# Performance work log

Measured on AMD Instinct MI355X. Metric: run time of the kernel, lower is better.

## Reference

```python
import jax, jax.numpy as jnp
import numpy as np

ALPHA = 1.702  # sigmoid-GLU scale
LIMIT = 7.0    # clamp limit
TOP_K = 2      # num_experts_per_tok


def setup_inputs() -> dict:
    key = jax.random.key(0)
    ks = jax.random.split(key, 4)
    B, S, H, E, I = 2, 1024, 1024, 8, 2048
    return {
        "hidden_states": jax.random.normal(ks[0], (B, S, H), jnp.float32),
        "router_weight": jax.random.normal(ks[1], (E, H), jnp.float32),
        "router_bias": jnp.zeros((E,), jnp.float32),
        "gate_up_proj": jax.random.normal(ks[2], (E, H, 2 * I), jnp.float32) * 0.02,
        "gate_up_bias": jnp.zeros((E, 2 * I), jnp.float32),
        "down_proj": jax.random.normal(ks[3], (E, I, H), jnp.float32) * 0.02,
        "down_bias": jnp.zeros((E, H), jnp.float32),
    }


def reference(hidden_states, router_weight, router_bias, gate_up_proj,
              gate_up_bias, down_proj, down_bias):
    B, S, H = hidden_states.shape
    E, _, two_I = gate_up_proj.shape
    I = two_I // 2

    flat = hidden_states.reshape(B * S, H)  # [T, H]

    # Router: softmax + top-k
    logits = flat @ router_weight.T + router_bias            # [T, E]
    scores = jax.nn.softmax(logits, axis=-1)
    topk_w, topk_idx = jax.lax.top_k(scores, TOP_K)          # [T, K]

    # Dense per-expert gated FFN (einsum 'abmh,ehn->abemn' computes all experts
    # on all tokens; the reshape/permute dance is a mathematical no-op).
    gu = jnp.einsum('th,ehn->ten', flat, gate_up_proj) + gate_up_bias  # [T, E, 2I]
    gate = jnp.minimum(gu[..., :I], LIMIT)
    up = jnp.clip(gu[..., I:], -LIMIT, LIMIT)
    glu = gate * jax.nn.sigmoid(gate * ALPHA)
    act = (up + 1.0) * glu                                   # [T, E, I]

    down = jnp.einsum('tei,eih->teh', act, down_proj) + down_bias  # [T, E, H]

    # Combine: gather each token's top-k expert outputs, weighted sum.
    gathered = jnp.take_along_axis(down, topk_idx[:, :, None], axis=1)  # [T, K, H]
    out = (gathered * topk_w[:, :, None]).sum(axis=1)        # [T, H]
    return out.reshape(B, S, H)
```

## Files before the change

### kernel.cpp

```cpp
#include <hip/hip_runtime.h>
#include <math.h>

#define TT 2048
#define HH 1024
#define EE 8
#define II 2048
#define N1 4096
#define ALPHA 1.702f
#define LIMIT 7.0f

typedef __attribute__((ext_vector_type(8))) short short8;
typedef __attribute__((ext_vector_type(4))) float floatx4;

__device__ __forceinline__ short f2bf(float f) {
  union { float f; unsigned u; } v; v.f = f;
  unsigned r = (v.u + 0x7fffu + ((v.u >> 16) & 1u)) >> 16;
  return (short)r;
}
__device__ __forceinline__ float bf2f(unsigned short s) {
  union { unsigned u; float f; } v; v.u = ((unsigned)s) << 16;
  return v.f;
}

__global__ __launch_bounds__(256) void router_kernel(
    const float* __restrict__ x, const float* __restrict__ rw,
    const float* __restrict__ rb, int* __restrict__ topk_idx,
    float* __restrict__ topk_w) {
  const int t = blockIdx.x;
  const float* xr = x + (size_t)t * HH;
  const int lane = threadIdx.x & 63;
  const int wave = threadIdx.x >> 6;
  float xv[16];
#pragma unroll
  for (int i = 0; i < 16; i++) xv[i] = xr[lane + i * 64];
  __shared__ float logits[EE];
#pragma unroll
  for (int ee = 0; ee < 2; ee++) {
    const int e = wave * 2 + ee;
    const float* wr = rw + (size_t)e * HH;
    float s = 0.f;
#pragma unroll
    for (int i = 0; i < 16; i++) s += xv[i] * wr[lane + i * 64];
#pragma unroll
    for (int off = 32; off > 0; off >>= 1) s += __shfl_down(s, off, 64);
    if (lane == 0) logits[e] = s + rb[e];
  }
  __syncthreads();
  if (threadIdx.x == 0) {
    float l[EE], sc[EE];
    float mx = -3.4e38f;
    for (int i = 0; i < EE; i++) { l[i] = logits[i]; mx = fmaxf(mx, l[i]); }
    float sum = 0.f;
    for (int i = 0; i < EE; i++) { sc[i] = expf(l[i] - mx); sum += sc[i]; }
    const float inv = 1.f / sum;
    int i0 = 0;
    for (int i = 1; i < EE; i++) if (sc[i] > sc[i0]) i0 = i;
    int i1 = (i0 == 0) ? 1 : 0;
    for (int i = 0; i < EE; i++) if (i != i0 && sc[i] > sc[i1]) i1 = i;
    topk_idx[t * 2 + 0] = i0;
    topk_idx[t * 2 + 1] = i1;
    topk_w[t * 2 + 0] = sc[i0] * inv;
    topk_w[t * 2 + 1] = sc[i1] * inv;
  }
}

__global__ void assign_kernel(const int* __restrict__ topk_idx,
                              int* __restrict__ counts, int* __restrict__ rows) {
  const int id = blockIdx.x * blockDim.x + threadIdx.x;
  if (id >= TT * 2) return;
  const int e = topk_idx[id];
  const int slot = atomicAdd(&counts[e], 1);
  rows[e * TT + slot] = id;
}

__global__ __launch_bounds__(256) void gemm_gu(
    const float* __restrict__ x, const float* __restrict__ gup,
    const float* __restrict__ gub, const int* __restrict__ counts,
    const int* __restrict__ rows, unsigned short* __restrict__ gu) {
  const int e = blockIdx.z, mtile = blockIdx.y, ntile = blockIdx.x;
  const int count = counts[e];
  if (mtile * 128 >= count) return;
  const int* rl = rows + e * TT + mtile * 128;
  __shared__ short As[128][40];
  __shared__ short Bs[128][40];
  const int tid = threadIdx.x;
  const int lane = tid & 63, wave = tid >> 6;
  const int wm = (wave & 1) << 6, wn = (wave >> 1) << 6;
  const int quad = lane >> 4, r16 = lane & 15;

  const int arow = tid >> 2, akoct = tid & 3;
  const int cr0 = (mtile * 128 + arow < count) ? arow : (count - 1 - mtile * 128);
  const int cr1 = (mtile * 128 + arow + 64 < count) ? arow + 64 : (count - 1 - mtile * 128);
  const float* a0 = x + (size_t)(rl[cr0] >> 1) * HH;
  const float* a1 = x + (size_t)(rl[cr1] >> 1) * HH;

  const int bn = tid & 127, bk = tid >> 7;
  const float* bb = gup + (size_t)e * HH * N1 + ntile * 128 + bn;

  floatx4 acc[4][4] = {};

  for (int k0 = 0; k0 < HH; k0 += 32) {
    __syncthreads();
    {
      const float4* p = (const float4*)(a0 + k0 + akoct * 8);
      float4 v0 = p[0], v1 = p[1];
      short8 s;
      s[0]=f2bf(v0.x); s[1]=f2bf(v0.y); s[2]=f2bf(v0.z); s[3]=f2bf(v0.w);
      s[4]=f2bf(v1.x); s[5]=f2bf(v1.y); s[6]=f2bf(v1.z); s[7]=f2bf(v1.w);
      *(short8*)&As[arow][akoct * 8] = s;
      p = (const float4*)(a1 + k0 + akoct * 8);
      v0 = p[0]; v1 = p[1];
      s[0]=f2bf(v0.x); s[1]=f2bf(v0.y); s[2]=f2bf(v0.z); s[3]=f2bf(v0.w);
      s[4]=f2bf(v1.x); s[5]=f2bf(v1.y); s[6]=f2bf(v1.z); s[7]=f2bf(v1.w);
      *(short8*)&As[arow + 64][akoct * 8] = s;
    }
    {
      const float* p = bb + (size_t)(k0 + bk * 8) * N1;
      short8 s;
#pragma unroll
      for (int j = 0; j < 8; j++) s[j] = f2bf(p[(size_t)j * N1]);
      *(short8*)&Bs[bn][bk * 8] = s;
      p = bb + (size_t)(k0 + (bk + 2) * 8) * N1;
#pragma unroll
      for (int j = 0; j < 8; j++) s[j] = f2bf(p[(size_t)j * N1]);
      *(short8*)&Bs[bn][(bk + 2) * 8] = s;
    }
    __syncthreads();
    short8 af[4], bf_[4];
#pragma unroll
    for (int i = 0; i < 4; i++)
      af[i] = *(const short8*)&As[wm + i * 16 + r16][quad * 8];
#pragma unroll
    for (int j = 0; j < 4; j++)
      bf_[j] = *(const short8*)&Bs[wn + j * 16 + r16][quad * 8];
#pragma unroll
    for (int i = 0; i < 4; i++)
#pragma unroll
      for (int j = 0; j < 4; j++)
        acc[i][j] = __builtin_amdgcn_mfma_f32_16x16x32_bf16(af[i], bf_[j], acc[i][j], 0, 0, 0);
  }
#pragma unroll
  for (int i = 0; i < 4; i++) {
#pragma unroll
    for (int reg = 0; reg < 4; reg++) {
      const int rrow = wm + i * 16 + quad * 4 + reg;
      if (mtile * 128 + rrow < count) {
        const int ent = rl[rrow];
        unsigned short* orow = gu + (size_t)ent * N1 + ntile * 128;
#pragma unroll
        for (int j = 0; j < 4; j++) {
          const int c = wn + j * 16 + r16;
          const float v = acc[i][j][reg] + gub[e * N1 + ntile * 128 + c];
          orow[c] = (unsigned short)f2bf(v);
        }
      }
    }
  }
}

__global__ void act_kernel(const unsigned short* __restrict__ gu,
                           unsigned short* __restrict__ act) {
  const int id = blockIdx.x * blockDim.x + threadIdx.x;
  if (id >= TT * 2 * II) return;
  const int r = id >> 11;
  const int i = id & (II - 1);
  float g = bf2f(gu[(size_t)r * N1 + i]);
  float u = bf2f(gu[(size_t)r * N1 + II + i]);
  g = fminf(g, LIMIT);
  u = fminf(fmaxf(u, -LIMIT), LIMIT);
  const float glu = g / (1.f + expf(-g * ALPHA));
  act[(size_t)r * II + i] = (unsigned short)f2bf((u + 1.f) * glu);
}

__global__ __launch_bounds__(256) void gemm_down(
    const unsigned short* __restrict__ act, const float* __restrict__ dp,
    const float* __restrict__ db, const int* __restrict__ counts,
    const int* __restrict__ rows, float* __restrict__ dout) {
  const int e = blockIdx.z, mtile = blockIdx.y, ntile = blockIdx.x;
  const int count = counts[e];
  if (mtile * 128 >= count) return;
  const int* rl = rows + e * TT + mtile * 128;
  __shared__ short As[128][40];
  __shared__ short Bs[128][40];
  const int tid = threadIdx.x;
  const int lane = tid & 63, wave = tid >> 6;
  const int wm = (wave & 1) << 6, wn = (wave >> 1) << 6;
  const int quad = lane >> 4, r16 = lane & 15;

  const int arow = tid >> 2, akoct = tid & 3;
  const int cr0 = (mtile * 128 + arow < count) ? arow : (count - 1 - mtile * 128);
  const int cr1 = (mtile * 128 + arow + 64 < count) ? arow + 64 : (count - 1 - mtile * 128);
  const unsigned short* a0 = act + (size_t)rl[cr0] * II;
  const unsigned short* a1 = act + (size_t)rl[cr1] * II;

  const int bn = tid & 127, bk = tid >> 7;
  const float* bb = dp + (size_t)e * II * HH + ntile * 128 + bn;

  floatx4 acc[4][4] = {};

  for (int k0 = 0; k0 < II; k0 += 32) {
    __syncthreads();
    {
      *(short8*)&As[arow][akoct * 8] = *(const short8*)(a0 + k0 + akoct * 8);
      *(short8*)&As[arow + 64][akoct * 8] = *(const short8*)(a1 + k0 + akoct * 8);
    }
    {
      const float* p = bb + (size_t)(k0 + bk * 8) * HH;
      short8 s;
#pragma unroll
      for (int j = 0; j < 8; j++) s[j] = f2bf(p[(size_t)j * HH]);
      *(short8*)&Bs[bn][bk * 8] = s;
      p = bb + (size_t)(k0 + (bk + 2) * 8) * HH;
#pragma unroll
      for (int j = 0; j < 8; j++) s[j] = f2bf(p[(size_t)j * HH]);
      *(short8*)&Bs[bn][(bk + 2) * 8] = s;
    }
    __syncthreads();
    short8 af[4], bf_[4];
#pragma unroll
    for (int i = 0; i < 4; i++)
      af[i] = *(const short8*)&As[wm + i * 16 + r16][quad * 8];
#pragma unroll
    for (int j = 0; j < 4; j++)
      bf_[j] = *(const short8*)&Bs[wn + j * 16 + r16][quad * 8];
#pragma unroll
    for (int i = 0; i < 4; i++)
#pragma unroll
      for (int j = 0; j < 4; j++)
        acc[i][j] = __builtin_amdgcn_mfma_f32_16x16x32_bf16(af[i], bf_[j], acc[i][j], 0, 0, 0);
  }
#pragma unroll
  for (int i = 0; i < 4; i++) {
#pragma unroll
    for (int reg = 0; reg < 4; reg++) {
      const int rrow = wm + i * 16 + quad * 4 + reg;
      if (mtile * 128 + rrow < count) {
        const int ent = rl[rrow];
        float* orow = dout + (size_t)ent * HH + ntile * 128;
#pragma unroll
        for (int j = 0; j < 4; j++) {
          const int c = wn + j * 16 + r16;
          orow[c] = acc[i][j][reg] + db[e * HH + ntile * 128 + c];
        }
      }
    }
  }
}

__global__ void combine_kernel(const float* __restrict__ dout,
                               const float* __restrict__ tw,
                               float* __restrict__ out) {
  const int id = blockIdx.x * blockDim.x + threadIdx.x;
  const int t = id >> 8;
  const int h = (id & 255) * 4;
  const float w0 = tw[t * 2], w1 = tw[t * 2 + 1];
  const float4 a = *(const float4*)(dout + (size_t)(2 * t) * HH + h);
  const float4 b = *(const float4*)(dout + (size_t)(2 * t + 1) * HH + h);
  float4 o;
  o.x = w0 * a.x + w1 * b.x;
  o.y = w0 * a.y + w1 * b.y;
  o.z = w0 * a.z + w1 * b.z;
  o.w = w0 * a.w + w1 * b.w;
  *(float4*)(out + (size_t)t * HH + h) = o;
}

extern "C" void kernel_launch(void* const* d_in, const int* in_sizes, int n_in,
                              void* d_out, int out_size, void* d_ws, size_t ws_size,
                              hipStream_t stream) {
  const float* x   = (const float*)d_in[0];
  const float* rw  = (const float*)d_in[1];
  const float* rb  = (const float*)d_in[2];
  const float* gup = (const float*)d_in[3];
  const float* gub = (const float*)d_in[4];
  const float* dp  = (const float*)d_in[5];
  const float* db  = (const float*)d_in[6];
  float* out = (float*)d_out;

  char* ws = (char*)d_ws;
  int*   topk_idx = (int*)(ws + 0);
  float* topk_w   = (float*)(ws + 16384);
  int*   counts   = (int*)(ws + 32768);
  int*   rows     = (int*)(ws + 33024);
  unsigned short* gu  = (unsigned short*)(ws + 131072);
  unsigned short* act = (unsigned short*)(ws + 131072 + 33554432);
  float* dout = (float*)(ws + 131072 + 33554432 + 16777216);

  router_kernel<<<TT, 256, 0, stream>>>(x, rw, rb, topk_idx, topk_w);
  hipMemsetAsync(counts, 0, 64, stream);
  assign_kernel<<<(TT * 2 + 255) / 256, 256, 0, stream>>>(topk_idx, counts, rows);
  gemm_gu<<<dim3(N1 / 128, TT / 128, EE), 256, 0, stream>>>(x, gup, gub, counts, rows, gu);
  act_kernel<<<(TT * 2 * II) / 256, 256, 0, stream>>>(gu, act);
  gemm_down<<<dim3(HH / 128, TT / 128, EE), 256, 0, stream>>>(act, dp, db, counts, rows, dout);
  combine_kernel<<<(TT * HH / 4) / 256, 256, 0, stream>>>(dout, topk_w, out);
}
```

Measured before the change: 454.3 us.

## Double-buffer GEMM loads in registers, use 512-thread blocks, split-K down GEMM

Both expert GEMMs now use 512-thread blocks with eight waves, each computing a 64x32 sub-tile. They prefetch the next K slice into registers while the current slice is staged in LDS, and they convert fp32 to bf16 with the packed v_cvt_pk_bf16_f32 instruction. The down GEMM is split into two K halves that write separate partial buffers, reusing the free gu region for the second one, and the combine kernel adds the two halves. The activation kernel is vectorised to process eight elements per thread. The aim is more parallelism and latency hiding, paid for with higher register pressure, an extra partial buffer read in combine, and more blocks in the down GEMM.

```diff
diff --git a/kernel.cpp b/kernel.cpp
--- a/kernel.cpp
+++ b/kernel.cpp
@@ -11,6 +11,7 @@
 
 typedef __attribute__((ext_vector_type(8))) short short8;
 typedef __attribute__((ext_vector_type(4))) float floatx4;
+typedef __attribute__((ext_vector_type(4))) unsigned int uintx4;
 
 __device__ __forceinline__ short f2bf(float f) {
   union { float f; unsigned u; } v; v.f = f;
@@ -20,6 +21,11 @@
 __device__ __forceinline__ float bf2f(unsigned short s) {
   union { unsigned u; float f; } v; v.u = ((unsigned)s) << 16;
   return v.f;
+}
+__device__ __forceinline__ unsigned cvt2(float lo, float hi) {
+  unsigned r;
+  asm("v_cvt_pk_bf16_f32 %0, %1, %2" : "=v"(r) : "v"(lo), "v"(hi));
+  return r;
 }
 
 __global__ __launch_bounds__(256) void router_kernel(
@@ -73,7 +79,7 @@
   rows[e * TT + slot] = id;
 }
 
-__global__ __launch_bounds__(256) void gemm_gu(
+__global__ __launch_bounds__(512, 4) void gemm_gu(
     const float* __restrict__ x, const float* __restrict__ gup,
     const float* __restrict__ gub, const int* __restrict__ counts,
     const int* __restrict__ rows, unsigned short* __restrict__ gu) {
@@ -85,58 +91,55 @@
   __shared__ short Bs[128][40];
   const int tid = threadIdx.x;
   const int lane = tid & 63, wave = tid >> 6;
-  const int wm = (wave & 1) << 6, wn = (wave >> 1) << 6;
+  const int wm = (wave & 1) << 6, wn = (wave >> 1) << 5;
   const int quad = lane >> 4, r16 = lane & 15;
 
   const int arow = tid >> 2, akoct = tid & 3;
-  const int cr0 = (mtile * 128 + arow < count) ? arow : (count - 1 - mtile * 128);
-  const int cr1 = (mtile * 128 + arow + 64 < count) ? arow + 64 : (count - 1 - mtile * 128);
-  const float* a0 = x + (size_t)(rl[cr0] >> 1) * HH;
-  const float* a1 = x + (size_t)(rl[cr1] >> 1) * HH;
-
-  const int bn = tid & 127, bk = tid >> 7;
-  const float* bb = gup + (size_t)e * HH * N1 + ntile * 128 + bn;
-
-  floatx4 acc[4][4] = {};
+  const int cr = (mtile * 128 + arow < count) ? arow : (count - 1 - mtile * 128);
+  const float* ap = x + (size_t)(rl[cr] >> 1) * HH + akoct * 8;
+
+  const int bn = tid & 127, bko = tid >> 7;
+  const float* bp = gup + (size_t)e * HH * N1 + (size_t)bko * 8 * N1 + ntile * 128 + bn;
+
+  floatx4 acc[4][2] = {};
+
+  float4 va0 = ((const float4*)ap)[0];
+  float4 va1 = ((const float4*)ap)[1];
+  float vb[8];
+#pragma unroll
+  for (int j = 0; j < 8; j++) vb[j] = bp[(size_t)j * N1];
+  ap += 32;
+  bp += (size_t)32 * N1;
 
   for (int k0 = 0; k0 < HH; k0 += 32) {
     __syncthreads();
-    {
-      const float4* p = (const float4*)(a0 + k0 + akoct * 8);
-      float4 v0 = p[0], v1 = p[1];
-      short8 s;
-      s[0]=f2bf(v0.x); s[1]=f2bf(v0.y); s[2]=f2bf(v0.z); s[3]=f2bf(v0.w);
-      s[4]=f2bf(v1.x); s[5]=f2bf(v1.y); s[6]=f2bf(v1.z); s[7]=f2bf(v1.w);
-      *(short8*)&As[arow][akoct * 8] = s;
-      p = (const float4*)(a1 + k0 + akoct * 8);
-      v0 = p[0]; v1 = p[1];
-      s[0]=f2bf(v0.x); s[1]=f2bf(v0.y); s[2]=f2bf(v0.z); s[3]=f2bf(v0.w);
-      s[4]=f2bf(v1.x); s[5]=f2bf(v1.y); s[6]=f2bf(v1.z); s[7]=f2bf(v1.w);
-      *(short8*)&As[arow + 64][akoct * 8] = s;
-    }
-    {
-      const float* p = bb + (size_t)(k0 + bk * 8) * N1;
-      short8 s;
-#pragma unroll
-      for (int j = 0; j < 8; j++) s[j] = f2bf(p[(size_t)j * N1]);
-      *(short8*)&Bs[bn][bk * 8] = s;
-      p = bb + (size_t)(k0 + (bk + 2) * 8) * N1;
-#pragma unroll
-      for (int j = 0; j < 8; j++) s[j] = f2bf(p[(size_t)j * N1]);
-      *(short8*)&Bs[bn][(bk + 2) * 8] = s;
+    uintx4 aw, bw;
+    aw[0] = cvt2(va0.x, va0.y); aw[1] = cvt2(va0.z, va0.w);
+    aw[2] = cvt2(va1.x, va1.y); aw[3] = cvt2(va1.z, va1.w);
+    bw[0] = cvt2(vb[0], vb[1]); bw[1] = cvt2(vb[2], vb[3]);
+    bw[2] = cvt2(vb[4], vb[5]); bw[3] = cvt2(vb[6], vb[7]);
+    *(uintx4*)&As[arow][akoct * 8] = aw;
+    *(uintx4*)&Bs[bn][bko * 8] = bw;
+    if (k0 + 32 < HH) {
+      va0 = ((const float4*)ap)[0];
+      va1 = ((const float4*)ap)[1];
+#pragma unroll
+      for (int j = 0; j < 8; j++) vb[j] = bp[(size_t)j * N1];
+      ap += 32;
+      bp += (size_t)32 * N1;
     }
     __syncthreads();
-    short8 af[4], bf_[4];
+    short8 af[4], bf_[2];
 #pragma unroll
     for (int i = 0; i < 4; i++)
       af[i] = *(const short8*)&As[wm + i * 16 + r16][quad * 8];
 #pragma unroll
-    for (int j = 0; j < 4; j++)
+    for (int j = 0; j < 2; j++)
       bf_[j] = *(const short8*)&Bs[wn + j * 16 + r16][quad * 8];
 #pragma unroll
     for (int i = 0; i < 4; i++)
 #pragma unroll
-      for (int j = 0; j < 4; j++)
+      for (int j = 0; j < 2; j++)
         acc[i][j] = __builtin_amdgcn_mfma_f32_16x16x32_bf16(af[i], bf_[j], acc[i][j], 0, 0, 0);
   }
 #pragma unroll
@@ -148,7 +151,7 @@
         const int ent = rl[rrow];
         unsigned short* orow = gu + (size_t)ent * N1 + ntile * 128;
 #pragma unroll
-        for (int j = 0; j < 4; j++) {
+        for (int j = 0; j < 2; j++) {
           const int c = wn + j * 16 + r16;
           const float v = acc[i][j][reg] + gub[e * N1 + ntile * 128 + c];
           orow[c] = (unsigned short)f2bf(v);
@@ -161,74 +164,86 @@
 __global__ void act_kernel(const unsigned short* __restrict__ gu,
                            unsigned short* __restrict__ act) {
   const int id = blockIdx.x * blockDim.x + threadIdx.x;
-  if (id >= TT * 2 * II) return;
-  const int r = id >> 11;
-  const int i = id & (II - 1);
-  float g = bf2f(gu[(size_t)r * N1 + i]);
-  float u = bf2f(gu[(size_t)r * N1 + II + i]);
-  g = fminf(g, LIMIT);
-  u = fminf(fmaxf(u, -LIMIT), LIMIT);
-  const float glu = g / (1.f + expf(-g * ALPHA));
-  act[(size_t)r * II + i] = (unsigned short)f2bf((u + 1.f) * glu);
-}
-
-__global__ __launch_bounds__(256) void gemm_down(
+  const int r = id >> 8;
+  const int i8 = (id & 255) * 8;
+  short8 g8 = *(const short8*)(gu + (size_t)r * N1 + i8);
+  short8 u8 = *(const short8*)(gu + (size_t)r * N1 + II + i8);
+  short8 o;
+#pragma unroll
+  for (int j = 0; j < 8; j++) {
+    float g = bf2f((unsigned short)g8[j]);
+    float u = bf2f((unsigned short)u8[j]);
+    g = fminf(g, LIMIT);
+    u = fminf(fmaxf(u, -LIMIT), LIMIT);
+    const float glu = g / (1.f + expf(-g * ALPHA));
+    o[j] = f2bf((u + 1.f) * glu);
+  }
+  *(short8*)(act + (size_t)r * II + i8) = o;
+}
+
+__global__ __launch_bounds__(512, 4) void gemm_down(
     const unsigned short* __restrict__ act, const float* __restrict__ dp,
     const float* __restrict__ db, const int* __restrict__ counts,
-    const int* __restrict__ rows, float* __restrict__ dout) {
-  const int e = blockIdx.z, mtile = blockIdx.y, ntile = blockIdx.x;
+    const int* __restrict__ rows, float* __restrict__ dout0,
+    float* __restrict__ dout1) {
+  const int e = blockIdx.z >> 1, kc = blockIdx.z & 1;
+  const int mtile = blockIdx.y, ntile = blockIdx.x;
   const int count = counts[e];
   if (mtile * 128 >= count) return;
+  const int kb = kc * (II / 2);
   const int* rl = rows + e * TT + mtile * 128;
   __shared__ short As[128][40];
   __shared__ short Bs[128][40];
   const int tid = threadIdx.x;
   const int lane = tid & 63, wave = tid >> 6;
-  const int wm = (wave & 1) << 6, wn = (wave >> 1) << 6;
+  const int wm = (wave & 1) << 6, wn = (wave >> 1) << 5;
   const int quad = lane >> 4, r16 = lane & 15;
 
   const int arow = tid >> 2, akoct = tid & 3;
-  const int cr0 = (mtile * 128 + arow < count) ? arow : (count - 1 - mtile * 128);
-  const int cr1 = (mtile * 128 + arow + 64 < count) ? arow + 64 : (count - 1 - mtile * 128);
-  const unsigned short* a0 = act + (size_t)rl[cr0] * II;
-  const unsigned short* a1 = act + (size_t)rl[cr1] * II;
-
-  const int bn = tid & 127, bk = tid >> 7;
-  const float* bb = dp + (size_t)e * II * HH + ntile * 128 + bn;
-
-  floatx4 acc[4][4] = {};
-
-  for (int k0 = 0; k0 < II; k0 += 32) {
+  const int cr = (mtile * 128 + arow < count) ? arow : (count - 1 - mtile * 128);
+  const unsigned short* ap = act + (size_t)rl[cr] * II + kb + akoct * 8;
+
+  const int bn = tid & 127, bko = tid >> 7;
+  const float* bp = dp + (size_t)e * II * HH + (size_t)(kb + bko * 8) * HH + ntile * 128 + bn;
+
+  floatx4 acc[4][2] = {};
+
+  short8 va = *(const short8*)ap;
+  float vb[8];
+#pragma unroll
+  for (int j = 0; j < 8; j++) vb[j] = bp[(size_t)j * HH];
+  ap += 32;
+  bp += (size_t)32 * HH;
+
+  for (int k0 = 0; k0 < II / 2; k0 += 32) {
     __syncthreads();
-    {
-      *(short8*)&As[arow][akoct * 8] = *(const short8*)(a0 + k0 + akoct * 8);
-      *(short8*)&As[arow + 64][akoct * 8] = *(const short8*)(a1 + k0 + akoct * 8);
-    }
-    {
-      const float* p = bb + (size_t)(k0 + bk * 8) * HH;
-      short8 s;
-#pragma unroll
-      for (int j = 0; j < 8; j++) s[j] = f2bf(p[(size_t)j * HH]);
-      *(short8*)&Bs[bn][bk * 8] = s;
-      p = bb + (size_t)(k0 + (bk + 2) * 8) * HH;
-#pragma unroll
-      for (int j = 0; j < 8; j++) s[j] = f2bf(p[(size_t)j * HH]);
-      *(short8*)&Bs[bn][(bk + 2) * 8] = s;
+    uintx4 bw;
+    bw[0] = cvt2(vb[0], vb[1]); bw[1] = cvt2(vb[2], vb[3]);
+    bw[2] = cvt2(vb[4], vb[5]); bw[3] = cvt2(vb[6], vb[7]);
+    *(short8*)&As[arow][akoct * 8] = va;
+    *(uintx4*)&Bs[bn][bko * 8] = bw;
+    if (k0 + 32 < II / 2) {
+      va = *(const short8*)ap;
+#pragma unroll
+      for (int j = 0; j < 8; j++) vb[j] = bp[(size_t)j * HH];
+      ap += 32;
+      bp += (size_t)32 * HH;
     }
     __syncthreads();
-    short8 af[4], bf_[4];
+    short8 af[4], bf_[2];
 #pragma unroll
     for (int i = 0; i < 4; i++)
       af[i] = *(const short8*)&As[wm + i * 16 + r16][quad * 8];
 #pragma unroll
-    for (int j = 0; j < 4; j++)
+    for (int j = 0; j < 2; j++)
       bf_[j] = *(const short8*)&Bs[wn + j * 16 + r16][quad * 8];
 #pragma unroll
     for (int i = 0; i < 4; i++)
 #pragma unroll
-      for (int j = 0; j < 4; j++)
+      for (int j = 0; j < 2; j++)
         acc[i][j] = __builtin_amdgcn_mfma_f32_16x16x32_bf16(af[i], bf_[j], acc[i][j], 0, 0, 0);
   }
+  float* dc = kc ? dout1 : dout0;
 #pragma unroll
   for (int i = 0; i < 4; i++) {
 #pragma unroll
@@ -236,31 +251,38 @@
       const int rrow = wm + i * 16 + quad * 4 + reg;
       if (mtile * 128 + rrow < count) {
         const int ent = rl[rrow];
-        float* orow = dout + (size_t)ent * HH + ntile * 128;
-#pragma unroll
-        for (int j = 0; j < 4; j++) {
+        float* orow = dc + (size_t)ent * HH + ntile * 128;
+#pragma unroll
+        for (int j = 0; j < 2; j++) {
           const int c = wn + j * 16 + r16;
-          orow[c] = acc[i][j][reg] + db[e * HH + ntile * 128 + c];
+          float v = acc[i][j][reg];
+          if (kc == 0) v += db[e * HH + ntile * 128 + c];
+          orow[c] = v;
         }
       }
     }
   }
 }
 
-__global__ void combine_kernel(const float* __restrict__ dout,
+__global__ void combine_kernel(const float* __restrict__ d0,
+                               const float* __restrict__ d1,
                                const float* __restrict__ tw,
                                float* __restrict__ out) {
   const int id = blockIdx.x * blockDim.x + threadIdx.x;
   const int t = id >> 8;
   const int h = (id & 255) * 4;
   const float w0 = tw[t * 2], w1 = tw[t * 2 + 1];
-  const float4 a = *(const float4*)(dout + (size_t)(2 * t) * HH + h);
-  const float4 b = *(const float4*)(dout + (size_t)(2 * t + 1) * HH + h);
+  const size_t r0 = (size_t)(2 * t) * HH + h;
+  const size_t r1 = (size_t)(2 * t + 1) * HH + h;
+  const float4 a0 = *(const float4*)(d0 + r0);
+  const float4 a1 = *(const float4*)(d1 + r0);
+  const float4 b0 = *(const float4*)(d0 + r1);
+  const float4 b1 = *(const float4*)(d1 + r1);
   float4 o;
-  o.x = w0 * a.x + w1 * b.x;
-  o.y = w0 * a.y + w1 * b.y;
-  o.z = w0 * a.z + w1 * b.z;
-  o.w = w0 * a.w + w1 * b.w;
+  o.x = w0 * (a0.x + a1.x) + w1 * (b0.x + b1.x);
+  o.y = w0 * (a0.y + a1.y) + w1 * (b0.y + b1.y);
+  o.z = w0 * (a0.z + a1.z) + w1 * (b0.z + b1.z);
+  o.w = w0 * (a0.w + a1.w) + w1 * (b0.w + b1.w);
   *(float4*)(out + (size_t)t * HH + h) = o;
 }
 
@@ -283,13 +305,14 @@
   int*   rows     = (int*)(ws + 33024);
   unsigned short* gu  = (unsigned short*)(ws + 131072);
   unsigned short* act = (unsigned short*)(ws + 131072 + 33554432);
-  float* dout = (float*)(ws + 131072 + 33554432 + 16777216);
+  float* dout0 = (float*)(ws + 131072 + 33554432 + 16777216);
+  float* dout1 = (float*)(ws + 131072);
 
   router_kernel<<<TT, 256, 0, stream>>>(x, rw, rb, topk_idx, topk_w);
   hipMemsetAsync(counts, 0, 64, stream);
   assign_kernel<<<(TT * 2 + 255) / 256, 256, 0, stream>>>(topk_idx, counts, rows);
-  gemm_gu<<<dim3(N1 / 128, TT / 128, EE), 256, 0, stream>>>(x, gup, gub, counts, rows, gu);
-  act_kernel<<<(TT * 2 * II) / 256, 256, 0, stream>>>(gu, act);
-  gemm_down<<<dim3(HH / 128, TT / 128, EE), 256, 0, stream>>>(act, dp, db, counts, rows, dout);
-  combine_kernel<<<(TT * HH / 4) / 256, 256, 0, stream>>>(dout, topk_w, out);
-}
+  gemm_gu<<<dim3(N1 / 128, TT / 128, EE), 512, 0, stream>>>(x, gup, gub, counts, rows, gu);
+  act_kernel<<<(TT * 2 * II / 8) / 256, 256, 0, stream>>>(gu, act);
+  gemm_down<<<dim3(HH / 128, TT / 128, EE * 2), 512, 0, stream>>>(act, dp, db, counts, rows, dout0, dout1);
+  combine_kernel<<<(TT * HH / 4) / 256, 256, 0, stream>>>(dout0, dout1, topk_w, out);
+}
```

Result: faster. 399.7 us (-12.0%).
